# Performance work log

Hardware: AMD Instinct MI355X
Metric: run time of the kernel (lower is better)

The kernel has to match this reference:

```python
import jax, jax.numpy as jnp
import numpy as np

D_MODEL = 1024
N_HEAD = 16
HEAD_DIM = D_MODEL // N_HEAD  # 64
B, T = 2, 2048
ROPE_BASE = 10000.0


def _rotary_cos_sin(seq_len, head_dim, dtype):
    inv_freq = 1.0 / (ROPE_BASE ** (jnp.arange(0, head_dim, 2, dtype=jnp.float32) / head_dim))
    t = jnp.arange(seq_len, dtype=jnp.float32)
    freqs = jnp.outer(t, inv_freq)  # [T, head_dim//2]
    cos = jnp.cos(freqs).astype(dtype)[None, :, None, :]  # [1,T,1,hd/2]
    sin = jnp.sin(freqs).astype(dtype)[None, :, None, :]
    return cos, sin


def _apply_rotary(x, cos, sin):
    d = x.shape[3] // 2
    x1, x2 = x[..., :d], x[..., d:]
    y1 = x1 * cos + x2 * sin
    y2 = -x1 * sin + x2 * cos
    return jnp.concatenate([y1, y2], axis=3).astype(x.dtype)


def setup_inputs() -> dict:
    key = jax.random.key(0)
    ks = jax.random.split(key, 7)
    s = 1.0 / np.sqrt(D_MODEL)
    return {
        "x": jax.random.normal(ks[0], (B, T, D_MODEL), dtype=jnp.float32),
        "Wq": jax.random.normal(ks[1], (D_MODEL, D_MODEL), dtype=jnp.float32) * s,
        "Wk": jax.random.normal(ks[2], (D_MODEL, D_MODEL), dtype=jnp.float32) * s,
        "Wq2": jax.random.normal(ks[3], (D_MODEL, D_MODEL), dtype=jnp.float32) * s,
        "Wk2": jax.random.normal(ks[4], (D_MODEL, D_MODEL), dtype=jnp.float32) * s,
        "Wv": jax.random.normal(ks[5], (D_MODEL, D_MODEL), dtype=jnp.float32) * s,
        "Wproj": jax.random.normal(ks[6], (D_MODEL, D_MODEL), dtype=jnp.float32) * s,
    }


def reference(x, Wq, Wk, Wq2, Wk2, Wv, Wproj):
    Bx, Tx, C = x.shape
    H, Dh = N_HEAD, HEAD_DIM

    def proj(W):
        return (x @ W.T).reshape(Bx, Tx, H, Dh)  # [B,T,H,Dh]

    q, k, q2, k2, v = proj(Wq), proj(Wk), proj(Wq2), proj(Wk2), proj(Wv)

    cos, sin = _rotary_cos_sin(Tx, Dh, x.dtype)
    q = _apply_rotary(q, cos, sin)
    k = _apply_rotary(k, cos, sin)
    q2 = _apply_rotary(q2, cos, sin)
    k2 = _apply_rotary(k2, cos, sin)

    scores = jnp.einsum('bqhd,bkhd->bhqk', q, k)
    scores2 = jnp.einsum('bqhd,bkhd->bhqk', q2, k2)
    pattern = (scores / Dh) * (scores2 / Dh)  # bilinear, no softmax
    causal = jnp.tril(jnp.ones((Tx, Tx), dtype=bool))
    pattern = jnp.where(causal[None, None, :, :], pattern, 0.0)

    z = jnp.einsum('bhqk,bkhd->bhqd', pattern, v)  # [B,H,T,Dh]
    y = z.transpose(0, 2, 1, 3).reshape(Bx, Tx, C)
    return y @ Wproj.T
```

## Files before the change

kernel.cpp:

```cpp
#include <hip/hip_runtime.h>
#include <hip/hip_bf16.h>

#define TSEQ 2048
#define NHEAD 16
#define DM 1024
#define NBATCH 2
#define MTOK (NBATCH * TSEQ)

typedef __attribute__((ext_vector_type(8))) short short8;
typedef __attribute__((ext_vector_type(4))) float floatx4;
typedef __attribute__((address_space(1))) const void gvoid;
typedef __attribute__((address_space(3))) void lvoid;

static __device__ __forceinline__ unsigned short f2bf(float f) {
    unsigned int u = __float_as_uint(f);
    return (unsigned short)((u + 0x7fffu + ((u >> 16) & 1u)) >> 16);
}
static __device__ __forceinline__ float bf2f(unsigned short h) {
    return __uint_as_float(((unsigned int)h) << 16);
}

__global__ __launch_bounds__(256)
void pack_all_kernel(const float* __restrict__ x,
                     const float* __restrict__ w0, const float* __restrict__ w1,
                     const float* __restrict__ w2, const float* __restrict__ w3,
                     const float* __restrict__ w4, const float* __restrict__ w5,
                     unsigned short* __restrict__ dstX, unsigned short* __restrict__ dstW)
{
    const float* src;
    unsigned short* dst;
    int gid;
    bool ilv = false;
    if (blockIdx.x < 4096) {
        src = x; dst = dstX;
        gid = blockIdx.x * 256 + threadIdx.x;
    } else {
        int wi = (blockIdx.x - 4096) >> 10;
        const float* srcs[6] = {w0, w1, w2, w3, w4, w5};
        src = srcs[wi];
        dst = dstW + (size_t)wi * 1024 * 2048;
        gid = ((blockIdx.x - 4096) & 1023) * 256 + threadIdx.x;
        ilv = (wi >= 1 && wi <= 4);
    }
    int e   = gid * 4;
    int row = e >> 10;
    int col = e & 1023;
    float4 f = *(const float4*)(src + (size_t)row * 1024 + col);
    ushort4 hi;
    hi.x = f2bf(f.x);
    hi.y = f2bf(f.y);
    hi.z = f2bf(f.z);
    hi.w = f2bf(f.w);
    int drow = row;
    if (ilv) {
        int hh = row >> 6, d = row & 63;
        int dd = (d < 32) ? ((d >> 3) * 16 + (d & 7))
                          : (((d - 32) >> 3) * 16 + 8 + (d & 7));
        drow = hh * 64 + dd;
    }
    *(ushort4*)(dst + (size_t)drow * 2048 + col) = hi;
}

#define VMW(N) asm volatile("s_waitcnt vmcnt(" #N ")" ::: "memory")
#define LGKM0  asm volatile("s_waitcnt lgkmcnt(0)" ::: "memory")

__global__ __launch_bounds__(512, 2)
void gemm_qkv(const unsigned short* __restrict__ Ap,
              const unsigned short* __restrict__ Bp,
              unsigned short* __restrict__ Ch, unsigned short* __restrict__ Vt)
{
    __shared__ __align__(16) unsigned short A0s[2][8192];
    __shared__ __align__(16) unsigned short A1s[2][8192];
    __shared__ __align__(16) unsigned short B0s[2][10240];
    __shared__ __align__(16) unsigned short B1s[2][10240];

    const int t    = threadIdx.x;
    const int lane = t & 63;
    const int w    = t >> 6;
    const int wm   = w >> 2;
    const int wn   = w & 3;
    const int s    = lane & 15;
    const int g    = (lane >> 4) & 3;
    const int row0 = blockIdx.x * 256;
    const int col0 = blockIdx.y * 320;

    const int cofs  = ((g ^ ((lane >> 1) & 3)) << 3);
    const int addrA = (wm * 128 + s) * 32 + cofs;
    const int addrB = (wn * 80 + s) * 32 + cofs;

    const int alc = (t & 3) ^ ((t >> 3) & 3);
    const unsigned short* Ag = Ap + (size_t)(row0 + (t >> 2)) * 2048 + alc * 8;
    const unsigned short* Bg = Bp + (size_t)(col0 + (t >> 2)) * 2048 + alc * 8;

#define STAGE_A(dst, kofs) {                                                                              \
    __builtin_amdgcn_global_load_lds((gvoid*)(Ag + (kofs)),              (lvoid*)((dst) + t * 8),        16, 0, 0); \
    __builtin_amdgcn_global_load_lds((gvoid*)(Ag + (kofs) + 128 * 2048), (lvoid*)((dst) + 4096 + t * 8), 16, 0, 0); }

#define STAGE_B(dst, kofs) {                                                                              \
    __builtin_amdgcn_global_load_lds((gvoid*)(Bg + (kofs)),              (lvoid*)((dst) + t * 8),        16, 0, 0); \
    __builtin_amdgcn_global_load_lds((gvoid*)(Bg + (kofs) + 128 * 2048), (lvoid*)((dst) + 4096 + t * 8), 16, 0, 0); \
    if (t < 256)                                                                                          \
    __builtin_amdgcn_global_load_lds((gvoid*)(Bg + (kofs) + 256 * 2048), (lvoid*)((dst) + 8192 + t * 8), 16, 0, 0); }

    floatx4 acc[8][5];
    #pragma unroll
    for (int ii = 0; ii < 8; ++ii)
        #pragma unroll
        for (int nf = 0; nf < 5; ++nf)
            acc[ii][nf] = (floatx4)(0.0f);

    STAGE_A(A0s[0], 0);
    STAGE_B(B0s[0], 0);
    STAGE_A(A1s[0], 32);
    STAGE_B(B1s[0], 32);
    STAGE_A(A0s[1], 64);
    STAGE_B(B0s[1], 64);
    VMW(4);
    __builtin_amdgcn_s_barrier();
    __builtin_amdgcn_sched_barrier(0);

#define MFMA_CLUSTER(IOFS)                                                                      \
    __builtin_amdgcn_s_setprio(1);                                                              \
    _Pragma("unroll")                                                                           \
    for (int ii = 0; ii < 4; ++ii)                                                              \
        _Pragma("unroll")                                                                       \
        for (int nf = 0; nf < 5; ++nf)                                                          \
            acc[(IOFS) + ii][nf] = __builtin_amdgcn_mfma_f32_16x16x32_bf16(af[ii], bf[nf], acc[(IOFS) + ii][nf], 0, 0, 0); \
    __builtin_amdgcn_s_setprio(0);

#define TILE_BODY(TAU, DO12, DO34, W2, W4)                                                      \
{                                                                                               \
    const int cur_ = (TAU) & 1;                                                                 \
    const unsigned short* a0k = A0s[cur_];                                                      \
    const unsigned short* a1k = A1s[cur_];                                                      \
    const unsigned short* b0k = B0s[cur_];                                                      \
    const unsigned short* b1k = B1s[cur_];                                                      \
    short8 af[4], bf[5];                                                                        \
                             \
    _Pragma("unroll")                                                                           \
    for (int ii = 0; ii < 4; ++ii) af[ii] = *(const short8*)&a0k[addrA + ii * 512];             \
    _Pragma("unroll")                                                                           \
    for (int nf = 0; nf < 5; ++nf) bf[nf] = *(const short8*)&b0k[addrB + nf * 512];             \
    if (DO12) STAGE_A(A1s[cur_ ^ 1], ((TAU) + 1) * 64 + 32);                                    \
    LGKM0;                                                                                      \
    __builtin_amdgcn_s_barrier();                                                               \
    __builtin_amdgcn_sched_barrier(0);                                                          \
    MFMA_CLUSTER(0)                                                                             \
                                  \
    _Pragma("unroll")                                                                           \
    for (int ii = 0; ii < 4; ++ii) af[ii] = *(const short8*)&a0k[addrA + (ii + 4) * 512];       \
    if (DO12) STAGE_B(B1s[cur_ ^ 1], ((TAU) + 1) * 64 + 32);                                    \
    LGKM0;                                                                                      \
    W2;                                                                                         \
    __builtin_amdgcn_s_barrier();                                                               \
    __builtin_amdgcn_sched_barrier(0);                                                          \
    MFMA_CLUSTER(4)                                                                             \
                             \
    _Pragma("unroll")                                                                           \
    for (int ii = 0; ii < 4; ++ii) af[ii] = *(const short8*)&a1k[addrA + ii * 512];             \
    _Pragma("unroll")                                                                           \
    for (int nf = 0; nf < 5; ++nf) bf[nf] = *(const short8*)&b1k[addrB + nf * 512];             \
    if (DO34) STAGE_A(A0s[cur_], ((TAU) + 2) * 64);                                             \
    LGKM0;                                                                                      \
    __builtin_amdgcn_s_barrier();                                                               \
    __builtin_amdgcn_sched_barrier(0);                                                          \
    MFMA_CLUSTER(0)                                                                             \
                                  \
    _Pragma("unroll")                                                                           \
    for (int ii = 0; ii < 4; ++ii) af[ii] = *(const short8*)&a1k[addrA + (ii + 4) * 512];       \
    if (DO34) STAGE_B(B0s[cur_], ((TAU) + 2) * 64);                                             \
    LGKM0;                                                                                      \
    W4;                                                                                        \
    __builtin_amdgcn_s_barrier();                                                               \
    __builtin_amdgcn_sched_barrier(0);                                                          \
    MFMA_CLUSTER(4)                                                                             \
}

    #pragma unroll 2
    for (int tau = 0; tau < 14; ++tau)
        TILE_BODY(tau, 1, 1, VMW(8), VMW(8));
    TILE_BODY(14, 1, 0, VMW(8), VMW(4));
    TILE_BODY(15, 0, 0, VMW(0), ((void)0));

#undef TILE_BODY
#undef MFMA_CLUSTER
#undef STAGE_A
#undef STAGE_B

    const int cr = (lane >> 4) * 4;
    const int cc = lane & 15;
    const int rwbase = row0 + wm * 128;
    const float L2C = -0.41524101186092029f;

    #pragma unroll
    for (int nf = 0; nf < 5; ++nf) {
        const int cg = col0 + wn * 80 + nf * 16;
        const int p  = cg >> 10;
        const int h  = (cg >> 6) & 15;
        const int f  = (cg >> 4) & 3;
        if (p < 4) {
            const float sc  = (p == 0 || p == 2) ? 0.015625f : 1.0f;
            const float inv = exp2f((float)(f * 8 + (cc & 7)) * L2C);
            unsigned short* hp = Ch + (size_t)p * 4194304;
            #pragma unroll
            for (int ii = 0; ii < 8; ++ii) {
                int r0  = rwbase + ii * 16 + cr;
                int bhi = ((r0 >> 11) << 4) + h;
                size_t base = ((size_t)bhi * 2048 + (r0 & 2047)) * 64;
                #pragma unroll
                for (int rr = 0; rr < 4; ++rr) {
                    float tt = (float)((r0 + rr) & 2047);
                    float s0, c0;
                    __sincosf(tt * inv, &s0, &c0);
                    float x  = acc[ii][nf][rr];
                    float xp = __shfl_xor(x, 8, 64);
                    float y  = (cc < 8) ? (x * c0 + xp * s0) : (x * c0 - xp * s0);
                    hp[base + (size_t)rr * 64 + (f * 16 + cc)] = f2bf(y * sc);
                }
            }
        } else {
            #pragma unroll
            for (int ii = 0; ii < 8; ++ii) {
                int r0  = rwbase + ii * 16 + cr;
                int bhi = ((r0 >> 11) << 4) + h;
                int d   = f * 16 + cc;
                ushort4 o;
                o.x = f2bf(acc[ii][nf][0]); o.y = f2bf(acc[ii][nf][1]);
                o.z = f2bf(acc[ii][nf][2]); o.w = f2bf(acc[ii][nf][3]);
                *(ushort4*)(Vt + ((size_t)bhi * 64 + d) * 2048 + (r0 & 2047)) = o;
            }
        }
    }
}

__global__ __launch_bounds__(256)
void gemm_proj(const unsigned short* __restrict__ Ap,
               const unsigned short* __restrict__ Bp,
               float* __restrict__ Cf)
{
    __shared__ __align__(16) unsigned short Ah[128 * 32];
    __shared__ __align__(16) unsigned short Bh[128 * 32];

    const int t    = threadIdx.x;
    const int lane = t & 63;
    const int s    = lane & 15;
    const int row0 = blockIdx.x * 128;
    const int col0 = blockIdx.y * 128;
    const int m0   = ((t >> 6) >> 1) * 64;
    const int n0   = ((t >> 6) & 1) * 64;

    floatx4 acc[4][4];
    #pragma unroll
    for (int i = 0; i < 4; ++i)
        #pragma unroll
        for (int j = 0; j < 4; ++j)
            acc[i][j] = (floatx4)(0.0f);

    const int sr  = t >> 2;
    const int skx = ((t & 3) ^ ((t >> 3) & 3)) * 8;
    char* dA  = (char*)Ah + (size_t)t * 16;
    char* dB  = (char*)Bh + (size_t)t * 16;
    const size_t arow = (size_t)(row0 + sr) * 2048 + skx;
    const size_t brow = (size_t)(col0 + sr) * 2048 + skx;

    #define ISSUE(k0)                                                                         \
    {                                                                                         \
        const unsigned short* ga = Ap + arow + (k0);                                          \
        const unsigned short* gb = Bp + brow + (k0);                                          \
        __builtin_amdgcn_global_load_lds((gvoid*)ga,                 (lvoid*)dA,          16, 0, 0); \
        __builtin_amdgcn_global_load_lds((gvoid*)(ga + 64*2048),     (lvoid*)(dA + 4096), 16, 0, 0); \
        __builtin_amdgcn_global_load_lds((gvoid*)gb,                 (lvoid*)dB,          16, 0, 0); \
        __builtin_amdgcn_global_load_lds((gvoid*)(gb + 64*2048),     (lvoid*)(dB + 4096), 16, 0, 0); \
    }

    const int cofs = (((lane >> 4) ^ ((lane >> 1) & 3)) << 3);

    ISSUE(0);
    for (int ks = 0; ks < 32; ++ks) {
        __syncthreads();
        short8 ahf[4], bhf[4];
        #pragma unroll
        for (int i = 0; i < 4; ++i)
            ahf[i] = *(const short8*)&Ah[(m0 + i * 16 + s) * 32 + cofs];
        #pragma unroll
        for (int j = 0; j < 4; ++j)
            bhf[j] = *(const short8*)&Bh[(n0 + j * 16 + s) * 32 + cofs];
        #pragma unroll
        for (int i = 0; i < 4; ++i)
            #pragma unroll
            for (int j = 0; j < 4; ++j)
                acc[i][j] = __builtin_amdgcn_mfma_f32_16x16x32_bf16(ahf[i], bhf[j], acc[i][j], 0, 0, 0);
        __syncthreads();
        if (ks + 1 < 32) ISSUE((ks + 1) * 32);
    }
    #undef ISSUE

    const int cr = (lane >> 4) * 4;
    const int cc = lane & 15;
    #pragma unroll
    for (int i = 0; i < 4; ++i)
        #pragma unroll
        for (int j = 0; j < 4; ++j) {
            int r = row0 + m0 + i * 16 + cr;
            int c = col0 + n0 + j * 16 + cc;
            #pragma unroll
            for (int rr = 0; rr < 4; ++rr)
                Cf[(size_t)(r + rr) * 1024 + c] = acc[i][j][rr];
        }
}

__global__ __launch_bounds__(512, 2)
void attn_mfma(const unsigned short* __restrict__ qh, const unsigned short* __restrict__ q2h,
               const unsigned short* __restrict__ kh, const unsigned short* __restrict__ k2h,
               const unsigned short* __restrict__ vt, unsigned short* __restrict__ zout)
{
    __shared__ __align__(16) unsigned short smem[65536];
    unsigned short* qs  = smem;
    unsigned short* q2s = smem + 8192;
    unsigned short* psq = smem;
    unsigned short* kvb = smem + 16384;

    const int bid  = blockIdx.x;
    const int xcd  = bid & 7;
    const int slot = bid >> 3;
    const int hh   = slot >> 3;
    const int pr   = slot & 7;
    const int bh   = xcd * 4 + hh;
    const int t  = threadIdx.x;
    const int lane = t & 63;
    const int w    = t >> 6;
    const int s    = lane & 15;
    const int g    = lane >> 4;
    const int mk   = (w >> 1) * 32;
    const int nq   = (w & 1) * 64;

    const int b = bh >> 4, h = bh & 15;

    short8 kf[2], k2f[2], vf[2];

#define LOADKV(TK) {                                                                \
    const unsigned short* kb  = kh  + ((size_t)bh * 2048 + (TK) * 128) * 64;        \
    const unsigned short* k2b = k2h + ((size_t)bh * 2048 + (TK) * 128) * 64;        \
    const unsigned short* vb  = vt  + (size_t)bh * 131072 + (TK) * 128;             \
    const int krow_ = t >> 2;                                                       \
    const int vd_   = t >> 3;                                                       \
    _Pragma("unroll")                                                               \
    for (int c = 0; c < 2; ++c) {                                                   \
        int cg_ = (t & 3) * 2 + c;                                                  \
        kf[c]  = *(const short8*)(kb  + (size_t)krow_ * 64 + cg_ * 8);              \
        k2f[c] = *(const short8*)(k2b + (size_t)krow_ * 64 + cg_ * 8);              \
        int cg16_ = (t & 7) * 2 + c;                                                \
        vf[c]  = *(const short8*)(vb + (size_t)vd_ * 2048 + cg16_ * 8);             \
    } }

#define WRITEKV(DST) {                                                              \
    unsigned short* ksd_  = (DST);                                                  \
    unsigned short* k2sd_ = (DST) + 8192;                                           \
    unsigned short* vtsd_ = (DST) + 16384;                                          \
    const int krow_ = t >> 2;                                                       \
    const int vd_   = t >> 3;                                                       \
    _Pragma("unroll")                                                               \
    for (int c = 0; c < 2; ++c) {                                                   \
        int cg_  = (t & 3) * 2 + c;                                                 \
        int cgm_ = (cg_ + krow_) & 7;                                               \
        *(short8*)&ksd_ [krow_ * 64 + cgm_ * 8] = kf[c];                            \
        *(short8*)&k2sd_[krow_ * 64 + cgm_ * 8] = k2f[c];                           \
        int cg16_  = (t & 7) * 2 + c;                                               \
        int cgm16_ = (cg16_ + vd_) & 15;                                            \
        *(short8*)&vtsd_[vd_ * 128 + cgm16_ * 8] = vf[c];                           \
    } }

    #pragma unroll
    for (int pass = 0; pass < 2; ++pass) {
        const int qt = pass ? pr : (15 - pr);

        __syncthreads();

        LOADKV(0);

        {
            const unsigned short* qb  = qh  + ((size_t)bh * 2048 + qt * 128) * 64;
            const unsigned short* q2b = q2h + ((size_t)bh * 2048 + qt * 128) * 64;
            const int row = t >> 2;
            #pragma unroll
            for (int c = 0; c < 2; ++c) {
                int cg  = (t & 3) * 2 + c;
                short8 a  = *(const short8*)(qb  + (size_t)row * 64 + cg * 8);
                short8 a2 = *(const short8*)(q2b + (size_t)row * 64 + cg * 8);
                int cgm = (cg + row) & 7;
                *(short8*)&qs [row * 64 + cgm * 8] = a;
                *(short8*)&q2s[row * 64 + cgm * 8] = a2;
            }
        }
        __syncthreads();
        short8 bq[2][4], bq2[2][4];
        #pragma unroll
        for (int kstep = 0; kstep < 2; ++kstep) {
            const int gl = kstep * 4 + g;
            #pragma unroll
            for (int j = 0; j < 4; ++j) {
                int row = nq + j * 16 + s;
                int a = row * 64 + ((gl + row) & 7) * 8;
                bq[kstep][j]  = *(const short8*)&qs [a];
                bq2[kstep][j] = *(const short8*)&q2s[a];
            }
        }

        WRITEKV(kvb);
        if (qt > 0) LOADKV(1);
        __syncthreads();

        floatx4 zac[4];
        #pragma unroll
        for (int j = 0; j < 4; ++j)
            zac[j] = (floatx4)(0.0f);

        for (int tk = 0; tk <= qt; ++tk) {
            const int cur = tk & 1;
            unsigned short* kvc = kvb + cur * 24576;
            unsigned short* kvn = kvb + (cur ^ 1) * 24576;

            if (tk < qt) WRITEKV(kvn);

            #pragma unroll
            for (int i = 0; i < 2; ++i) {
                floatx4 a1[4], a2[4];
                #pragma unroll
                for (int j = 0; j < 4; ++j) { a1[j] = (floatx4)(0.0f); a2[j] = (floatx4)(0.0f); }
                #pragma unroll
                for (int kstep = 0; kstep < 2; ++kstep) {
                    const int gl = kstep * 4 + g;
                    int row = mk + i * 16 + s;
                    int a = row * 64 + ((gl + row) & 7) * 8;
                    short8 ak  = *(const short8*)&kvc[a];
                    short8 ak2 = *(const short8*)&kvc[8192 + a];
                    #pragma unroll
                    for (int j = 0; j < 4; ++j) {
                        a1[j] = __builtin_amdgcn_mfma_f32_16x16x32_bf16(ak,  bq[kstep][j],  a1[j], 0, 0, 0);
                        a2[j] = __builtin_amdgcn_mfma_f32_16x16x32_bf16(ak2, bq2[kstep][j], a2[j], 0, 0, 0);
                    }
                }
                const int kl0   = mk + i * 16 + g * 4;
                const int chunk = kl0 >> 3;
                const int sub   = kl0 & 7;
                if (tk < qt) {
                    #pragma unroll
                    for (int j = 0; j < 4; ++j) {
                        const int ql = nq + j * 16 + s;
                        ushort4 pw;
                        pw.x = f2bf(a1[j][0] * a2[j][0]);
                        pw.y = f2bf(a1[j][1] * a2[j][1]);
                        pw.z = f2bf(a1[j][2] * a2[j][2]);
                        pw.w = f2bf(a1[j][3] * a2[j][3]);
                        *(ushort4*)&psq[ql * 128 + ((chunk + ql) & 15) * 8 + sub] = pw;
                    }
                } else {
                    #pragma unroll
                    for (int j = 0; j < 4; ++j) {
                        const int ql = nq + j * 16 + s;
                        ushort4 pw;
                        pw.x = (kl0 + 0 <= ql) ? f2bf(a1[j][0] * a2[j][0]) : (unsigned short)0;
                        pw.y = (kl0 + 1 <= ql) ? f2bf(a1[j][1] * a2[j][1]) : (unsigned short)0;
                        pw.z = (kl0 + 2 <= ql) ? f2bf(a1[j][2] * a2[j][2]) : (unsigned short)0;
                        pw.w = (kl0 + 3 <= ql) ? f2bf(a1[j][3] * a2[j][3]) : (unsigned short)0;
                        *(ushort4*)&psq[ql * 128 + ((chunk + ql) & 15) * 8 + sub] = pw;
                    }
                }
            }

            __syncthreads();

            if (tk + 2 <= qt) LOADKV(tk + 2);
            __builtin_amdgcn_sched_barrier(0);

            const int wm0 = w * 16;
            #pragma unroll
            for (int kstep = 0; kstep < 4; ++kstep) {
                const int cbase = kstep * 4 + g;
                short8 ap, bv[4];
                {
                    int q = wm0 + s;
                    ap = *(const short8*)&psq[q * 128 + ((cbase + q) & 15) * 8];
                }
                #pragma unroll
                for (int jd = 0; jd < 4; ++jd) {
                    int d = jd * 16 + s;
                    bv[jd] = *(const short8*)&kvc[16384 + d * 128 + ((cbase + d) & 15) * 8];
                }
                #pragma unroll
                for (int jd = 0; jd < 4; ++jd)
                    zac[jd] = __builtin_amdgcn_mfma_f32_16x16x32_bf16(ap, bv[jd], zac[jd], 0, 0, 0);
            }

            __syncthreads();
        }

        const size_t zrow0 = (size_t)(b * TSEQ + qt * 128);
        #pragma unroll
        for (int j = 0; j < 4; ++j)
            #pragma unroll
            for (int r = 0; r < 4; ++r) {
                size_t row = zrow0 + w * 16 + g * 4 + r;
                int col = h * 64 + j * 16 + s;
                zout[row * 2048 + col] = f2bf(zac[j][r]);
            }
    }
#undef LOADKV
#undef WRITEKV
}

extern "C" void kernel_launch(void* const* d_in, const int* in_sizes, int n_in,
                              void* d_out, int out_size, void* d_ws, size_t ws_size,
                              hipStream_t stream)
{
    const float* x     = (const float*)d_in[0];
    const float* Wq    = (const float*)d_in[1];
    const float* Wk    = (const float*)d_in[2];
    const float* Wq2   = (const float*)d_in[3];
    const float* Wk2   = (const float*)d_in[4];
    const float* Wv    = (const float*)d_in[5];
    const float* Wproj = (const float*)d_in[6];

    unsigned short* Xp    = (unsigned short*)d_ws;
    unsigned short* Wp    = (unsigned short*)((char*)d_ws + 16777216);
    unsigned short* heads = (unsigned short*)((char*)d_ws + 41943040);
    unsigned short* vt    = (unsigned short*)((char*)d_ws + 75497472);

    const size_t HS = (size_t)32 * 2048 * 64;
    unsigned short* qh  = heads;
    unsigned short* kh  = heads + 1 * HS;
    unsigned short* q2h = heads + 2 * HS;
    unsigned short* k2h = heads + 3 * HS;

    pack_all_kernel<<<10240, 256, 0, stream>>>(x, Wproj, Wq, Wk, Wq2, Wk2, Wv, Xp, Wp);
    gemm_qkv<<<dim3(16, 16), 512, 0, stream>>>(Xp, Wp + (size_t)1024 * 2048, heads, vt);
    attn_mfma<<<256, 512, 0, stream>>>(qh, q2h, kh, k2h, vt, Xp);
    gemm_proj<<<dim3(32, 8), 256, 0, stream>>>(Xp, Wp, (float*)d_out);
}
```

Before: 202.2 us.

## Split attention blocks per query tile and drop LDS double buffering

The attention kernel no longer has one block handle two query tiles (a long and a short one) in sequence. Each block now handles a single tile, with twice as many blocks launched. The LDS K/K2/V double buffer becomes a single buffer, cutting shared memory from 128KB to 80KB, with only a register-staged prefetch of the next tile. The aim is more parallelism and possibly better occupancy, at the cost of an extra barrier per iteration and less overlap between LDS writes and compute. Dropping the paired scheduling may also bring back load imbalance across the causal tiles.

```diff
diff --git a/kernel.cpp b/kernel.cpp
--- a/kernel.cpp
+++ b/kernel.cpp
@@ -314,18 +314,23 @@
                const unsigned short* __restrict__ kh, const unsigned short* __restrict__ k2h,
                const unsigned short* __restrict__ vt, unsigned short* __restrict__ zout)
 {
-    __shared__ __align__(16) unsigned short smem[65536];
+    __shared__ __align__(16) unsigned short smem[40960];
     unsigned short* qs  = smem;
     unsigned short* q2s = smem + 8192;
     unsigned short* psq = smem;
-    unsigned short* kvb = smem + 16384;
+    unsigned short* ks  = smem + 16384;
+    unsigned short* k2s = smem + 24576;
+    unsigned short* vts = smem + 32768;
 
     const int bid  = blockIdx.x;
-    const int xcd  = bid & 7;
-    const int slot = bid >> 3;
+    const int half = bid >> 8;
+    const int r    = bid & 255;
+    const int xcd  = r & 7;
+    const int slot = r >> 3;
     const int hh   = slot >> 3;
     const int pr   = slot & 7;
     const int bh   = xcd * 4 + hh;
+    const int qt   = half ? pr : (15 - pr);
     const int t  = threadIdx.x;
     const int lane = t & 63;
     const int w    = t >> 6;
@@ -353,160 +358,140 @@
         vf[c]  = *(const short8*)(vb + (size_t)vd_ * 2048 + cg16_ * 8);             \
     } }
 
-#define WRITEKV(DST) {                                                              \
-    unsigned short* ksd_  = (DST);                                                  \
-    unsigned short* k2sd_ = (DST) + 8192;                                           \
-    unsigned short* vtsd_ = (DST) + 16384;                                          \
-    const int krow_ = t >> 2;                                                       \
-    const int vd_   = t >> 3;                                                       \
-    _Pragma("unroll")                                                               \
-    for (int c = 0; c < 2; ++c) {                                                   \
-        int cg_  = (t & 3) * 2 + c;                                                 \
-        int cgm_ = (cg_ + krow_) & 7;                                               \
-        *(short8*)&ksd_ [krow_ * 64 + cgm_ * 8] = kf[c];                            \
-        *(short8*)&k2sd_[krow_ * 64 + cgm_ * 8] = k2f[c];                           \
-        int cg16_  = (t & 7) * 2 + c;                                               \
-        int cgm16_ = (cg16_ + vd_) & 15;                                            \
-        *(short8*)&vtsd_[vd_ * 128 + cgm16_ * 8] = vf[c];                           \
-    } }
-
-    #pragma unroll
-    for (int pass = 0; pass < 2; ++pass) {
-        const int qt = pass ? pr : (15 - pr);
-
+    LOADKV(0);
+
+    {
+        const unsigned short* qb  = qh  + ((size_t)bh * 2048 + qt * 128) * 64;
+        const unsigned short* q2b = q2h + ((size_t)bh * 2048 + qt * 128) * 64;
+        const int row = t >> 2;
+        #pragma unroll
+        for (int c = 0; c < 2; ++c) {
+            int cg  = (t & 3) * 2 + c;
+            short8 a  = *(const short8*)(qb  + (size_t)row * 64 + cg * 8);
+            short8 a2 = *(const short8*)(q2b + (size_t)row * 64 + cg * 8);
+            int cgm = (cg + row) & 7;
+            *(short8*)&qs [row * 64 + cgm * 8] = a;
+            *(short8*)&q2s[row * 64 + cgm * 8] = a2;
+        }
+    }
+    __syncthreads();
+    short8 bq[2][4], bq2[2][4];
+    #pragma unroll
+    for (int kstep = 0; kstep < 2; ++kstep) {
+        const int gl = kstep * 4 + g;
+        #pragma unroll
+        for (int j = 0; j < 4; ++j) {
+            int row = nq + j * 16 + s;
+            int a = row * 64 + ((gl + row) & 7) * 8;
+            bq[kstep][j]  = *(const short8*)&qs [a];
+            bq2[kstep][j] = *(const short8*)&q2s[a];
+        }
+    }
+
+    floatx4 zac[4];
+    #pragma unroll
+    for (int j = 0; j < 4; ++j)
+        zac[j] = (floatx4)(0.0f);
+
+    for (int tk = 0; tk <= qt; ++tk) {
         __syncthreads();
-
-        LOADKV(0);
-
         {
-            const unsigned short* qb  = qh  + ((size_t)bh * 2048 + qt * 128) * 64;
-            const unsigned short* q2b = q2h + ((size_t)bh * 2048 + qt * 128) * 64;
-            const int row = t >> 2;
+            const int krow = t >> 2;
+            const int vd   = t >> 3;
             #pragma unroll
             for (int c = 0; c < 2; ++c) {
                 int cg  = (t & 3) * 2 + c;
-                short8 a  = *(const short8*)(qb  + (size_t)row * 64 + cg * 8);
-                short8 a2 = *(const short8*)(q2b + (size_t)row * 64 + cg * 8);
-                int cgm = (cg + row) & 7;
-                *(short8*)&qs [row * 64 + cgm * 8] = a;
-                *(short8*)&q2s[row * 64 + cgm * 8] = a2;
+                int cgm = (cg + krow) & 7;
+                *(short8*)&ks [krow * 64 + cgm * 8] = kf[c];
+                *(short8*)&k2s[krow * 64 + cgm * 8] = k2f[c];
+                int cg16  = (t & 7) * 2 + c;
+                int cgm16 = (cg16 + vd) & 15;
+                *(short8*)&vts[vd * 128 + cgm16 * 8] = vf[c];
             }
         }
         __syncthreads();
-        short8 bq[2][4], bq2[2][4];
-        #pragma unroll
-        for (int kstep = 0; kstep < 2; ++kstep) {
-            const int gl = kstep * 4 + g;
-            #pragma unroll
-            for (int j = 0; j < 4; ++j) {
-                int row = nq + j * 16 + s;
+
+        if (tk < qt) LOADKV(tk + 1);
+        __builtin_amdgcn_sched_barrier(0);
+
+        #pragma unroll
+        for (int i = 0; i < 2; ++i) {
+            floatx4 a1[4], a2[4];
+            #pragma unroll
+            for (int j = 0; j < 4; ++j) { a1[j] = (floatx4)(0.0f); a2[j] = (floatx4)(0.0f); }
+            #pragma unroll
+            for (int kstep = 0; kstep < 2; ++kstep) {
+                const int gl = kstep * 4 + g;
+                int row = mk + i * 16 + s;
                 int a = row * 64 + ((gl + row) & 7) * 8;
-                bq[kstep][j]  = *(const short8*)&qs [a];
-                bq2[kstep][j] = *(const short8*)&q2s[a];
-            }
-        }
-
-        WRITEKV(kvb);
-        if (qt > 0) LOADKV(1);
+                short8 ak  = *(const short8*)&ks [a];
+                short8 ak2 = *(const short8*)&k2s[a];
+                #pragma unroll
+                for (int j = 0; j < 4; ++j) {
+                    a1[j] = __builtin_amdgcn_mfma_f32_16x16x32_bf16(ak,  bq[kstep][j],  a1[j], 0, 0, 0);
+                    a2[j] = __builtin_amdgcn_mfma_f32_16x16x32_bf16(ak2, bq2[kstep][j], a2[j], 0, 0, 0);
+                }
+            }
+            const int kl0   = mk + i * 16 + g * 4;
+            const int chunk = kl0 >> 3;
+            const int sub   = kl0 & 7;
+            if (tk < qt) {
+                #pragma unroll
+                for (int j = 0; j < 4; ++j) {
+                    const int ql = nq + j * 16 + s;
+                    ushort4 pw;
+                    pw.x = f2bf(a1[j][0] * a2[j][0]);
+                    pw.y = f2bf(a1[j][1] * a2[j][1]);
+                    pw.z = f2bf(a1[j][2] * a2[j][2]);
+                    pw.w = f2bf(a1[j][3] * a2[j][3]);
+                    *(ushort4*)&psq[ql * 128 + ((chunk + ql) & 15) * 8 + sub] = pw;
+                }
+            } else {
+                #pragma unroll
+                for (int j = 0; j < 4; ++j) {
+                    const int ql = nq + j * 16 + s;
+                    ushort4 pw;
+                    pw.x = (kl0 + 0 <= ql) ? f2bf(a1[j][0] * a2[j][0]) : (unsigned short)0;
+                    pw.y = (kl0 + 1 <= ql) ? f2bf(a1[j][1] * a2[j][1]) : (unsigned short)0;
+                    pw.z = (kl0 + 2 <= ql) ? f2bf(a1[j][2] * a2[j][2]) : (unsigned short)0;
+                    pw.w = (kl0 + 3 <= ql) ? f2bf(a1[j][3] * a2[j][3]) : (unsigned short)0;
+                    *(ushort4*)&psq[ql * 128 + ((chunk + ql) & 15) * 8 + sub] = pw;
+                }
+            }
+        }
+
         __syncthreads();
 
-        floatx4 zac[4];
-        #pragma unroll
-        for (int j = 0; j < 4; ++j)
-            zac[j] = (floatx4)(0.0f);
-
-        for (int tk = 0; tk <= qt; ++tk) {
-            const int cur = tk & 1;
-            unsigned short* kvc = kvb + cur * 24576;
-            unsigned short* kvn = kvb + (cur ^ 1) * 24576;
-
-            if (tk < qt) WRITEKV(kvn);
-
-            #pragma unroll
-            for (int i = 0; i < 2; ++i) {
-                floatx4 a1[4], a2[4];
-                #pragma unroll
-                for (int j = 0; j < 4; ++j) { a1[j] = (floatx4)(0.0f); a2[j] = (floatx4)(0.0f); }
-                #pragma unroll
-                for (int kstep = 0; kstep < 2; ++kstep) {
-                    const int gl = kstep * 4 + g;
-                    int row = mk + i * 16 + s;
-                    int a = row * 64 + ((gl + row) & 7) * 8;
-                    short8 ak  = *(const short8*)&kvc[a];
-                    short8 ak2 = *(const short8*)&kvc[8192 + a];
-                    #pragma unroll
-                    for (int j = 0; j < 4; ++j) {
-                        a1[j] = __builtin_amdgcn_mfma_f32_16x16x32_bf16(ak,  bq[kstep][j],  a1[j], 0, 0, 0);
-                        a2[j] = __builtin_amdgcn_mfma_f32_16x16x32_bf16(ak2, bq2[kstep][j], a2[j], 0, 0, 0);
-                    }
-                }
-                const int kl0   = mk + i * 16 + g * 4;
-                const int chunk = kl0 >> 3;
-                const int sub   = kl0 & 7;
-                if (tk < qt) {
-                    #pragma unroll
-                    for (int j = 0; j < 4; ++j) {
-                        const int ql = nq + j * 16 + s;
-                        ushort4 pw;
-                        pw.x = f2bf(a1[j][0] * a2[j][0]);
-                        pw.y = f2bf(a1[j][1] * a2[j][1]);
-                        pw.z = f2bf(a1[j][2] * a2[j][2]);
-                        pw.w = f2bf(a1[j][3] * a2[j][3]);
-                        *(ushort4*)&psq[ql * 128 + ((chunk + ql) & 15) * 8 + sub] = pw;
-                    }
-                } else {
-                    #pragma unroll
-                    for (int j = 0; j < 4; ++j) {
-                        const int ql = nq + j * 16 + s;
-                        ushort4 pw;
-                        pw.x = (kl0 + 0 <= ql) ? f2bf(a1[j][0] * a2[j][0]) : (unsigned short)0;
-                        pw.y = (kl0 + 1 <= ql) ? f2bf(a1[j][1] * a2[j][1]) : (unsigned short)0;
-                        pw.z = (kl0 + 2 <= ql) ? f2bf(a1[j][2] * a2[j][2]) : (unsigned short)0;
-                        pw.w = (kl0 + 3 <= ql) ? f2bf(a1[j][3] * a2[j][3]) : (unsigned short)0;
-                        *(ushort4*)&psq[ql * 128 + ((chunk + ql) & 15) * 8 + sub] = pw;
-                    }
-                }
-            }
-
-            __syncthreads();
-
-            if (tk + 2 <= qt) LOADKV(tk + 2);
-            __builtin_amdgcn_sched_barrier(0);
-
-            const int wm0 = w * 16;
-            #pragma unroll
-            for (int kstep = 0; kstep < 4; ++kstep) {
-                const int cbase = kstep * 4 + g;
-                short8 ap, bv[4];
-                {
-                    int q = wm0 + s;
-                    ap = *(const short8*)&psq[q * 128 + ((cbase + q) & 15) * 8];
-                }
-                #pragma unroll
-                for (int jd = 0; jd < 4; ++jd) {
-                    int d = jd * 16 + s;
-                    bv[jd] = *(const short8*)&kvc[16384 + d * 128 + ((cbase + d) & 15) * 8];
-                }
-                #pragma unroll
-                for (int jd = 0; jd < 4; ++jd)
-                    zac[jd] = __builtin_amdgcn_mfma_f32_16x16x32_bf16(ap, bv[jd], zac[jd], 0, 0, 0);
-            }
-
-            __syncthreads();
-        }
-
-        const size_t zrow0 = (size_t)(b * TSEQ + qt * 128);
-        #pragma unroll
-        for (int j = 0; j < 4; ++j)
-            #pragma unroll
-            for (int r = 0; r < 4; ++r) {
-                size_t row = zrow0 + w * 16 + g * 4 + r;
-                int col = h * 64 + j * 16 + s;
-                zout[row * 2048 + col] = f2bf(zac[j][r]);
-            }
-    }
+        const int wm0 = w * 16;
+        #pragma unroll
+        for (int kstep = 0; kstep < 4; ++kstep) {
+            const int cbase = kstep * 4 + g;
+            short8 ap, bv[4];
+            {
+                int q = wm0 + s;
+                ap = *(const short8*)&psq[q * 128 + ((cbase + q) & 15) * 8];
+            }
+            #pragma unroll
+            for (int jd = 0; jd < 4; ++jd) {
+                int d = jd * 16 + s;
+                bv[jd] = *(const short8*)&vts[d * 128 + ((cbase + d) & 15) * 8];
+            }
+            #pragma unroll
+            for (int jd = 0; jd < 4; ++jd)
+                zac[jd] = __builtin_amdgcn_mfma_f32_16x16x32_bf16(ap, bv[jd], zac[jd], 0, 0, 0);
+        }
+    }
+
+    const size_t zrow0 = (size_t)(b * TSEQ + qt * 128);
+    #pragma unroll
+    for (int j = 0; j < 4; ++j)
+        #pragma unroll
+        for (int r2 = 0; r2 < 4; ++r2) {
+            size_t row = zrow0 + w * 16 + g * 4 + r2;
+            int col = h * 64 + j * 16 + s;
+            zout[row * 2048 + col] = f2bf(zac[j][r2]);
+        }
 #undef LOADKV
-#undef WRITEKV
 }
 
 extern "C" void kernel_launch(void* const* d_in, const int* in_sizes, int n_in,
@@ -534,6 +519,6 @@
 
     pack_all_kernel<<<10240, 256, 0, stream>>>(x, Wproj, Wq, Wk, Wq2, Wk2, Wv, Xp, Wp);
     gemm_qkv<<<dim3(16, 16), 512, 0, stream>>>(Xp, Wp + (size_t)1024 * 2048, heads, vt);
-    attn_mfma<<<256, 512, 0, stream>>>(qh, q2h, kh, k2h, vt, Xp);
+    attn_mfma<<<512, 512, 0, stream>>>(qh, q2h, kh, k2h, vt, Xp);
     gemm_proj<<<dim3(32, 8), 256, 0, stream>>>(Xp, Wp, (float*)d_out);
 }
```

Result: slower. 219.9 us (+8.7%).
